# Kernel tuning notes

Hardware: AMD Instinct MI355X
Metric: run time of the kernel (lower is better)

The kernel has to match this reference:

```python
import jax, jax.numpy as jnp
import numpy as np

NUM_CODES = 1024
EMBED_DIM = 256
COMMITMENT_COST = 0.25


def setup_inputs() -> dict:
    key = jax.random.key(0)
    kz, kc = jax.random.split(key)
    z = jax.random.normal(kz, (131072, EMBED_DIM), dtype=jnp.float32)
    # codebook init matches nn.Embedding weight uniform_(-1/num_codes, 1/num_codes)
    codebook = jax.random.uniform(kc, (NUM_CODES, EMBED_DIM), dtype=jnp.float32,
                                  minval=-1.0 / NUM_CODES, maxval=1.0 / NUM_CODES)
    return {"z": z, "codebook": codebook}


def reference(z, codebook):
    # Squared-euclidean distances; argmin is identical to cdist (euclidean) argmin.
    z2 = jnp.sum(z * z, axis=-1, keepdims=True)            # [N, 1]
    c2 = jnp.sum(codebook * codebook, axis=-1)             # [K]
    d = z2 - 2.0 * (z @ codebook.T) + c2                   # [N, K]
    indices = jnp.argmin(d, axis=-1)                       # [N]
    zq = codebook[indices]                                 # [N, D] embedding lookup

    commitment_loss = COMMITMENT_COST * jnp.mean(
        (jax.lax.stop_gradient(zq) - z) ** 2)
    zq_st = z + jax.lax.stop_gradient(zq - z)              # straight-through
    residual = z - jax.lax.stop_gradient(zq)               # z - z_q.detach()

    counts = jnp.bincount(indices, length=NUM_CODES).astype(jnp.float32)
    avg_probs = counts / jnp.sum(counts)
    perplexity = jnp.exp(-jnp.sum(avg_probs * jnp.log(avg_probs + 1e-10)))

    return zq_st, residual, indices, commitment_loss, perplexity
```

## Files before the change

kernel.cpp:

```cpp
#include <hip/hip_runtime.h>
#include <math.h>

#define NR 131072
#define KC 1024
#define DD 256

#define ZQ_OFF  0
#define RES_OFF 33554432
#define IDX_OFF 67108864
#define LOSS_OFF 67239936
#define PERP_OFF 67239937

#define WS_CNT 0
#define WS_C2N 4096
#define WS_BSS 8192
#define WS_CBS 16384

#define MARG 5e-4f
#define CCAP 24

#define FM(x,y) __fmul_rn((x),(y))
#define FA(x,y) __fadd_rn((x),(y))

typedef __attribute__((ext_vector_type(8))) short bf16x8;
typedef __attribute__((ext_vector_type(4))) float f32x4;

static __device__ __forceinline__ unsigned short bf16h(float f) {
  unsigned int u = __float_as_uint(f);
  u += 0x7FFFu + ((u >> 16) & 1u);
  return (unsigned short)(u >> 16);
}

static __device__ __forceinline__ float np_sumsq128(const float* __restrict__ q) {
  float lane[16];
#pragma unroll
  for (int l = 0; l < 16; l++) {
    float s0 = FM(q[l +   0], q[l +   0]);
    float s1 = FM(q[l +  16], q[l +  16]);
    float s2 = FM(q[l +  32], q[l +  32]);
    float s3 = FM(q[l +  48], q[l +  48]);
    float s4 = FM(q[l +  64], q[l +  64]);
    float s5 = FM(q[l +  80], q[l +  80]);
    float s6 = FM(q[l +  96], q[l +  96]);
    float s7 = FM(q[l + 112], q[l + 112]);
    lane[l] = FA(FA(FA(s0, s1), FA(s2, s3)), FA(FA(s4, s5), FA(s6, s7)));
  }
#pragma unroll
  for (int h = 8; h >= 1; h >>= 1)
#pragma unroll
    for (int l = 0; l < 8; l++)
      if (l < h) lane[l] = FA(lane[l], lane[l + h]);
  return lane[0];
}

static __device__ __forceinline__ float np_sumsq256(const float* __restrict__ p) {
  return FA(np_sumsq128(p), np_sumsq128(p + 128));
}

__global__ void vqs_c2(const float* __restrict__ cb, float* __restrict__ c2n) {
  const int code = blockIdx.x * 256 + threadIdx.x;
  if (code < KC) c2n[code] = np_sumsq256(cb + (size_t)code * DD);
}

__global__ void vqs_cbsplit(const float* __restrict__ cb,
                            unsigned short* __restrict__ cbs) {
  const int g  = blockIdx.x * 256 + threadIdx.x;
  const int t  = g >> 9;
  const int gi = g & 511;
  const int kc = gi >> 6, q = (gi >> 4) & 3, c = gi & 15;
  const float* src = cb + (size_t)(t * 16 + c) * DD + kc * 32 + q * 8;
  unsigned int w[4];
#pragma unroll
  for (int p = 0; p < 4; p++)
    w[p] = (unsigned int)bf16h(src[p * 2]) |
           ((unsigned int)bf16h(src[p * 2 + 1]) << 16);
  *(uint4*)(cbs + (size_t)g * 8) = make_uint4(w[0], w[1], w[2], w[3]);
}

__global__ __launch_bounds__(256, 4) void vqs_main(
    const float* __restrict__ z, const float* __restrict__ cb,
    const unsigned short* __restrict__ cbs,
    const float* __restrict__ c2n,
    float* __restrict__ out, int* __restrict__ counts,
    double* __restrict__ bss) {
  __shared__ unsigned short ccode[128][CCAP];
  __shared__ float cd[128][CCAP];
  __shared__ int ccnt[128];
  __shared__ float m1row[128];
  __shared__ float z2s[128];
  __shared__ int rowidx[128];
  __shared__ __align__(16) float c2l[1024];
  __shared__ double wred[4];

  const int tid = threadIdx.x, wg = blockIdx.x;
  const int wv = tid >> 6, ln = tid & 63;
  const int rl = ln & 15;
  const int qk = ln >> 4;
  const int rowg0 = wg * 128 + wv * 32 + rl;

#pragma unroll
  for (int i = 0; i < 4; i++)
    ((float4*)c2l)[i * 64 + ln] = ((const float4*)c2n)[i * 64 + ln];
  if (ln < 32) ccnt[wv * 32 + ln] = 0;

  bf16x8 zH0[8], zH1[8];
#pragma unroll
  for (int kc = 0; kc < 8; kc++) {
    const float4* p0 = (const float4*)(z + (size_t)rowg0 * DD + kc * 32 + qk * 8);
    const float4* p1 = (const float4*)(z + (size_t)(rowg0 + 16) * DD + kc * 32 + qk * 8);
    const float4 a0 = p0[0], b0 = p0[1];
    const float4 a1 = p1[0], b1 = p1[1];
    zH0[kc][0] = (short)bf16h(a0.x); zH0[kc][1] = (short)bf16h(a0.y);
    zH0[kc][2] = (short)bf16h(a0.z); zH0[kc][3] = (short)bf16h(a0.w);
    zH0[kc][4] = (short)bf16h(b0.x); zH0[kc][5] = (short)bf16h(b0.y);
    zH0[kc][6] = (short)bf16h(b0.z); zH0[kc][7] = (short)bf16h(b0.w);
    zH1[kc][0] = (short)bf16h(a1.x); zH1[kc][1] = (short)bf16h(a1.y);
    zH1[kc][2] = (short)bf16h(a1.z); zH1[kc][3] = (short)bf16h(a1.w);
    zH1[kc][4] = (short)bf16h(b1.x); zH1[kc][5] = (short)bf16h(b1.y);
    zH1[kc][6] = (short)bf16h(b1.z); zH1[kc][7] = (short)bf16h(b1.w);
  }

  {
    const int gg = ln >> 4, l = ln & 15;
#pragma unroll 1
    for (int g4 = 0; g4 < 8; g4++) {
      const int rlcl = wv * 32 + g4 * 4 + gg;
      const float* q = z + (size_t)(wg * 128 + rlcl) * DD;
      float blk[2];
#pragma unroll
      for (int b = 0; b < 2; b++) {
        const float* qq = q + b * 128;
        const float s0 = FM(qq[l +   0], qq[l +   0]);
        const float s1 = FM(qq[l +  16], qq[l +  16]);
        const float s2 = FM(qq[l +  32], qq[l +  32]);
        const float s3 = FM(qq[l +  48], qq[l +  48]);
        const float s4 = FM(qq[l +  64], qq[l +  64]);
        const float s5 = FM(qq[l +  80], qq[l +  80]);
        const float s6 = FM(qq[l +  96], qq[l +  96]);
        const float s7 = FM(qq[l + 112], qq[l + 112]);
        float v = FA(FA(FA(s0, s1), FA(s2, s3)), FA(FA(s4, s5), FA(s6, s7)));
#pragma unroll
        for (int h = 8; h >= 1; h >>= 1) v = FA(v, __shfl_down(v, h, 16));
        blk[b] = v;
      }
      if (l == 0) z2s[rlcl] = FA(blk[0], blk[1]);
    }
  }

  const float z2v0 = z2s[wv * 32 + rl];
  const float z2v1 = z2s[wv * 32 + rl + 16];
  const int rw0 = wv * 32 + rl;

  float m10 = INFINITY, m11 = INFINITY;
#pragma unroll 2
  for (int t = 0; t < 64; t++) {
    bf16x8 aH[8];
#pragma unroll
    for (int kc = 0; kc < 8; kc++)
      aH[kc] = *(const bf16x8*)(cbs + (size_t)t * 4096 + kc * 512 + ln * 8);

    f32x4 accA = {0.f, 0.f, 0.f, 0.f}, accB = accA;
#pragma unroll
    for (int kc = 0; kc < 8; kc++) {
      accA = __builtin_amdgcn_mfma_f32_16x16x32_bf16(aH[kc], zH0[kc], accA, 0, 0, 0);
      accB = __builtin_amdgcn_mfma_f32_16x16x32_bf16(aH[kc], zH1[kc], accB, 0, 0, 0);
    }
    const float4 c2v4 = *(const float4*)&c2l[t * 16 + qk * 4];
    float dh0[4], dh1[4];
#pragma unroll
    for (int r = 0; r < 4; r++) {
      const float c2v = r == 0 ? c2v4.x : r == 1 ? c2v4.y : r == 2 ? c2v4.z : c2v4.w;
      dh0[r] = z2v0 - 2.f * accA[r] + c2v;
      dh1[r] = z2v1 - 2.f * accB[r] + c2v;
      m10 = fminf(m10, dh0[r]);
      m11 = fminf(m11, dh1[r]);
    }
    m10 = fminf(m10, __shfl_xor(m10, 16));
    m10 = fminf(m10, __shfl_xor(m10, 32));
    m11 = fminf(m11, __shfl_xor(m11, 16));
    m11 = fminf(m11, __shfl_xor(m11, 32));
#pragma unroll
    for (int r = 0; r < 4; r++) {
      if (dh0[r] <= m10 + MARG) {
        const int s = atomicAdd(&ccnt[rw0], 1);
        if (s < CCAP) {
          ccode[rw0][s] = (unsigned short)(t * 16 + qk * 4 + r);
          cd[rw0][s] = dh0[r];
        }
      }
      if (dh1[r] <= m11 + MARG) {
        const int s = atomicAdd(&ccnt[rw0 + 16], 1);
        if (s < CCAP) {
          ccode[rw0 + 16][s] = (unsigned short)(t * 16 + qk * 4 + r);
          cd[rw0 + 16][s] = dh1[r];
        }
      }
    }
  }

  if (qk == 0) { m1row[rw0] = m10; m1row[rw0 + 16] = m11; }

  if (ln < 32) {
    const int rwl = wv * 32 + ln;
    const int row = wg * 128 + rwl;
    const float mf = m1row[rwl] + MARG;
    const int nc = ccnt[rwl];
    int best;
    if (nc > CCAP) {
      const float* zr = z + (size_t)row * DD;
      const float z2r = z2s[rwl];
      float db = INFINITY; best = 0;
      for (int c = 0; c < KC; c++) {
        const float* cr = cb + (size_t)c * DD;
        float dot = 0.f;
#pragma unroll 8
        for (int k = 0; k < DD; k++) dot = __fmaf_rn(zr[k], cr[k], dot);
        const float t1 = 2.0f * dot;
        const float d = FA(FA(z2r, -t1), c2l[c]);
        if (d < db) { db = d; best = c; }
      }
    } else {
      int kept = 0, kcode = 0;
      for (int s = 0; s < nc; s++)
        if (cd[rwl][s] <= mf) { kept++; kcode = ccode[rwl][s]; }
      if (kept == 1) best = kcode;
      else {
        const float* zr = z + (size_t)row * DD;
        const float z2r = z2s[rwl];
        float db = INFINITY; int bi = 0x7FFFFFFF;
        for (int s = 0; s < nc; s++) {
          if (cd[rwl][s] > mf) continue;
          const int c = ccode[rwl][s];
          const float* cr = cb + (size_t)c * DD;
          float dot = 0.f;
#pragma unroll 8
          for (int k = 0; k < DD; k++) dot = __fmaf_rn(zr[k], cr[k], dot);
          const float t1 = 2.0f * dot;
          const float d = FA(FA(z2r, -t1), c2l[c]);
          if (d < db || (d == db && c < bi)) { db = d; bi = c; }
        }
        best = bi;
      }
    }
    rowidx[rwl] = best;
    atomicAdd(&counts[best], 1);
    out[IDX_OFF + row] = (float)best;
  }

  float ss = 0.f;
#pragma unroll 1
  for (int g = 0; g < 32; g += 8) {
    float4 r4b[8], q4b[8];
#pragma unroll
    for (int u = 0; u < 8; u++) {
      const int rlcl = wv * 32 + g + u;
      const size_t zrow = (size_t)(wg * 128 + rlcl) * DD;
      r4b[u] = ((const float4*)(z + zrow))[ln];
      q4b[u] = ((const float4*)(cb + (size_t)rowidx[rlcl] * DD))[ln];
    }
#pragma unroll
    for (int u = 0; u < 8; u++) {
      const int rlcl = wv * 32 + g + u;
      const size_t zrow = (size_t)(wg * 128 + rlcl) * DD;
      const float4 r4 = r4b[u];
      const float4 q4 = q4b[u];
      float4 stv, rsv; float dq;
      stv.x = r4.x + (q4.x - r4.x); rsv.x = r4.x - q4.x; dq = q4.x - r4.x; ss = fmaf(dq, dq, ss);
      stv.y = r4.y + (q4.y - r4.y); rsv.y = r4.y - q4.y; dq = q4.y - r4.y; ss = fmaf(dq, dq, ss);
      stv.z = r4.z + (q4.z - r4.z); rsv.z = r4.z - q4.z; dq = q4.z - r4.z; ss = fmaf(dq, dq, ss);
      stv.w = r4.w + (q4.w - r4.w); rsv.w = r4.w - q4.w; dq = q4.w - r4.w; ss = fmaf(dq, dq, ss);
      ((float4*)(out + ZQ_OFF  + zrow))[ln] = stv;
      ((float4*)(out + RES_OFF + zrow))[ln] = rsv;
    }
  }
  double dss = (double)ss;
  for (int o = 32; o; o >>= 1) dss += __shfl_down(dss, o, 64);
  if (ln == 0) wred[wv] = dss;
  __syncthreads();
  if (tid == 0) bss[wg] = wred[0] + wred[1] + wred[2] + wred[3];
}

__global__ void vqs_final(const int* __restrict__ counts,
                          const double* __restrict__ bss,
                          float* __restrict__ out) {
  __shared__ double red[256];
  const int t = threadIdx.x;
  double s = 0.0;
  for (int i = t; i < 1024; i += 256) s += bss[i];
  red[t] = s; __syncthreads();
  for (int s2 = 128; s2 > 0; s2 >>= 1) { if (t < s2) red[t] += red[t + s2]; __syncthreads(); }
  const double ssq = red[0];
  __syncthreads();
  double h = 0.0;
  for (int c = t; c < 1024; c += 256) {
    double p = (double)counts[c] / 131072.0;
    h += p * log(p + 1e-10);
  }
  red[t] = h; __syncthreads();
  for (int s2 = 128; s2 > 0; s2 >>= 1) { if (t < s2) red[t] += red[t + s2]; __syncthreads(); }
  if (t == 0) {
    out[LOSS_OFF] = (float)(0.25 * ssq / 33554432.0);
    out[PERP_OFF] = (float)exp(-red[0]);
  }
}

extern "C" void kernel_launch(void* const* d_in, const int* in_sizes, int n_in,
                              void* d_out, int out_size, void* d_ws, size_t ws_size,
                              hipStream_t stream) {
  const float* z;
  const float* cb;
  if (in_sizes[0] == NR * DD) { z = (const float*)d_in[0]; cb = (const float*)d_in[1]; }
  else                        { cb = (const float*)d_in[0]; z = (const float*)d_in[1]; }

  float* out = (float*)d_out;
  char* ws = (char*)d_ws;
  int*            counts = (int*)(ws + WS_CNT);
  float*          c2n    = (float*)(ws + WS_C2N);
  double*         bssp   = (double*)(ws + WS_BSS);
  unsigned short* cbs    = (unsigned short*)(ws + WS_CBS);

  hipMemsetAsync(counts, 0, 4096, stream);
  vqs_c2<<<4, 256, 0, stream>>>(cb, c2n);
  vqs_cbsplit<<<128, 256, 0, stream>>>(cb, cbs);
  vqs_main<<<NR / 128, 256, 0, stream>>>(z, cb, cbs, c2n, out, counts, bssp);
  vqs_final<<<1, 256, 0, stream>>>(counts, bssp, out);
}
```

Measured before the change: 305.5 us.

## Split output writing into a separate kernel after index computation

Moves the straight-through/residual output writes and the squared-error reduction out of the main distance/argmin kernel into a new kernel launched with 2048 blocks, passing indices through a workspace buffer. The aim is to keep the main kernel lean on registers and LDS, and to let the bandwidth-heavy store phase run at higher occupancy on its own. The cost is that z is read a second time from memory, plus an extra launch and an index round-trip.

```diff
diff --git a/kernel.cpp b/kernel.cpp
--- a/kernel.cpp
+++ b/kernel.cpp
@@ -13,8 +13,9 @@
 
 #define WS_CNT 0
 #define WS_C2N 4096
-#define WS_BSS 8192
-#define WS_CBS 16384
+#define WS_IDX 8192
+#define WS_BSS 532480
+#define WS_CBS 548864
 
 #define MARG 5e-4f
 #define CCAP 24
@@ -57,12 +58,12 @@
   return FA(np_sumsq128(p), np_sumsq128(p + 128));
 }
 
-__global__ void vqs_c2(const float* __restrict__ cb, float* __restrict__ c2n) {
+__global__ void vqt_c2(const float* __restrict__ cb, float* __restrict__ c2n) {
   const int code = blockIdx.x * 256 + threadIdx.x;
   if (code < KC) c2n[code] = np_sumsq256(cb + (size_t)code * DD);
 }
 
-__global__ void vqs_cbsplit(const float* __restrict__ cb,
+__global__ void vqt_cbsplit(const float* __restrict__ cb,
                             unsigned short* __restrict__ cbs) {
   const int g  = blockIdx.x * 256 + threadIdx.x;
   const int t  = g >> 9;
@@ -77,20 +78,18 @@
   *(uint4*)(cbs + (size_t)g * 8) = make_uint4(w[0], w[1], w[2], w[3]);
 }
 
-__global__ __launch_bounds__(256, 4) void vqs_main(
+__global__ __launch_bounds__(256, 4) void vqt_main(
     const float* __restrict__ z, const float* __restrict__ cb,
     const unsigned short* __restrict__ cbs,
     const float* __restrict__ c2n,
     float* __restrict__ out, int* __restrict__ counts,
-    double* __restrict__ bss) {
+    int* __restrict__ idxw) {
   __shared__ unsigned short ccode[128][CCAP];
   __shared__ float cd[128][CCAP];
   __shared__ int ccnt[128];
   __shared__ float m1row[128];
   __shared__ float z2s[128];
-  __shared__ int rowidx[128];
   __shared__ __align__(16) float c2l[1024];
-  __shared__ double wred[4];
 
   const int tid = threadIdx.x, wg = blockIdx.x;
   const int wv = tid >> 6, ln = tid & 63;
@@ -242,26 +241,33 @@
         best = bi;
       }
     }
-    rowidx[rwl] = best;
     atomicAdd(&counts[best], 1);
+    idxw[row] = best;
     out[IDX_OFF + row] = (float)best;
   }
+}
+
+__global__ __launch_bounds__(256) void vqt_out(
+    const float* __restrict__ z, const float* __restrict__ cb,
+    const int* __restrict__ idxw, float* __restrict__ out,
+    double* __restrict__ bss) {
+  __shared__ double wred[4];
+  const int wv = threadIdx.x >> 6, ln = threadIdx.x & 63;
+  const int rowbase = (blockIdx.x * 4 + wv) * 16;
 
   float ss = 0.f;
 #pragma unroll 1
-  for (int g = 0; g < 32; g += 8) {
+  for (int g = 0; g < 16; g += 8) {
     float4 r4b[8], q4b[8];
 #pragma unroll
     for (int u = 0; u < 8; u++) {
-      const int rlcl = wv * 32 + g + u;
-      const size_t zrow = (size_t)(wg * 128 + rlcl) * DD;
+      const size_t zrow = (size_t)(rowbase + g + u) * DD;
       r4b[u] = ((const float4*)(z + zrow))[ln];
-      q4b[u] = ((const float4*)(cb + (size_t)rowidx[rlcl] * DD))[ln];
+      q4b[u] = ((const float4*)(cb + (size_t)idxw[rowbase + g + u] * DD))[ln];
     }
 #pragma unroll
     for (int u = 0; u < 8; u++) {
-      const int rlcl = wv * 32 + g + u;
-      const size_t zrow = (size_t)(wg * 128 + rlcl) * DD;
+      const size_t zrow = (size_t)(rowbase + g + u) * DD;
       const float4 r4 = r4b[u];
       const float4 q4 = q4b[u];
       float4 stv, rsv; float dq;
@@ -277,16 +283,16 @@
   for (int o = 32; o; o >>= 1) dss += __shfl_down(dss, o, 64);
   if (ln == 0) wred[wv] = dss;
   __syncthreads();
-  if (tid == 0) bss[wg] = wred[0] + wred[1] + wred[2] + wred[3];
-}
-
-__global__ void vqs_final(const int* __restrict__ counts,
+  if (threadIdx.x == 0) bss[blockIdx.x] = wred[0] + wred[1] + wred[2] + wred[3];
+}
+
+__global__ void vqt_final(const int* __restrict__ counts,
                           const double* __restrict__ bss,
                           float* __restrict__ out) {
   __shared__ double red[256];
   const int t = threadIdx.x;
   double s = 0.0;
-  for (int i = t; i < 1024; i += 256) s += bss[i];
+  for (int i = t; i < 2048; i += 256) s += bss[i];
   red[t] = s; __syncthreads();
   for (int s2 = 128; s2 > 0; s2 >>= 1) { if (t < s2) red[t] += red[t + s2]; __syncthreads(); }
   const double ssq = red[0];
@@ -316,12 +322,14 @@
   char* ws = (char*)d_ws;
   int*            counts = (int*)(ws + WS_CNT);
   float*          c2n    = (float*)(ws + WS_C2N);
+  int*            idxw   = (int*)(ws + WS_IDX);
   double*         bssp   = (double*)(ws + WS_BSS);
   unsigned short* cbs    = (unsigned short*)(ws + WS_CBS);
 
   hipMemsetAsync(counts, 0, 4096, stream);
-  vqs_c2<<<4, 256, 0, stream>>>(cb, c2n);
-  vqs_cbsplit<<<128, 256, 0, stream>>>(cb, cbs);
-  vqs_main<<<NR / 128, 256, 0, stream>>>(z, cb, cbs, c2n, out, counts, bssp);
-  vqs_final<<<1, 256, 0, stream>>>(counts, bssp, out);
-}
+  vqt_c2<<<4, 256, 0, stream>>>(cb, c2n);
+  vqt_cbsplit<<<128, 256, 0, stream>>>(cb, cbs);
+  vqt_main<<<NR / 128, 256, 0, stream>>>(z, cb, cbs, c2n, out, counts, idxw);
+  vqt_out<<<2048, 256, 0, stream>>>(z, cb, idxw, out, bssp);
+  vqt_final<<<1, 256, 0, stream>>>(counts, bssp, out);
+}
```

Result: slower. 333.2 us (+9.0%).

## Double-buffer codebook tiles in LDS via async global_load_lds

Applied to the files above, without the earlier changes.

Codebook bf16 tiles are prefetched one iteration ahead into per-wave double-buffered LDS using global_load_lds, with explicit vmcnt waits, instead of loading directly into registers each iteration. Launch bounds drop to one block per SIMD-group target and the loop is no longer unrolled. The intent is to hide L2 latency of codebook fetches behind MFMA work. It costs 64 KB of extra LDS per block, which sharply lowers occupancy.

```diff
diff --git a/kernel.cpp b/kernel.cpp
--- a/kernel.cpp
+++ b/kernel.cpp
@@ -29,6 +29,12 @@
   unsigned int u = __float_as_uint(f);
   u += 0x7FFFu + ((u >> 16) & 1u);
   return (unsigned short)(u >> 16);
+}
+
+static __device__ __forceinline__ void glds16(const void* g, void* l) {
+  __builtin_amdgcn_global_load_lds(
+      (const __attribute__((address_space(1))) void*)g,
+      (__attribute__((address_space(3))) void*)l, 16, 0, 0);
 }
 
 static __device__ __forceinline__ float np_sumsq128(const float* __restrict__ q) {
@@ -57,12 +63,12 @@
   return FA(np_sumsq128(p), np_sumsq128(p + 128));
 }
 
-__global__ void vqs_c2(const float* __restrict__ cb, float* __restrict__ c2n) {
+__global__ void vqA_c2(const float* __restrict__ cb, float* __restrict__ c2n) {
   const int code = blockIdx.x * 256 + threadIdx.x;
   if (code < KC) c2n[code] = np_sumsq256(cb + (size_t)code * DD);
 }
 
-__global__ void vqs_cbsplit(const float* __restrict__ cb,
+__global__ void vqA_cbsplit(const float* __restrict__ cb,
                             unsigned short* __restrict__ cbs) {
   const int g  = blockIdx.x * 256 + threadIdx.x;
   const int t  = g >> 9;
@@ -77,12 +83,13 @@
   *(uint4*)(cbs + (size_t)g * 8) = make_uint4(w[0], w[1], w[2], w[3]);
 }
 
-__global__ __launch_bounds__(256, 4) void vqs_main(
+__global__ __launch_bounds__(256, 1) void vqA_main(
     const float* __restrict__ z, const float* __restrict__ cb,
     const unsigned short* __restrict__ cbs,
     const float* __restrict__ c2n,
     float* __restrict__ out, int* __restrict__ counts,
     double* __restrict__ bss) {
+  __shared__ __align__(16) unsigned short ct[4][2][4096];
   __shared__ unsigned short ccode[128][CCAP];
   __shared__ float cd[128][CCAP];
   __shared__ int ccnt[128];
@@ -97,6 +104,16 @@
   const int rl = ln & 15;
   const int qk = ln >> 4;
   const int rowg0 = wg * 128 + wv * 32 + rl;
+
+#define STG(T, B) do {                                                        \
+    _Pragma("unroll")                                                         \
+    for (int kc_ = 0; kc_ < 8; kc_++) {                                       \
+      glds16(cbs + (size_t)(T) * 4096 + kc_ * 512 + ln * 8,                   \
+             &ct[wv][B][kc_ * 512]);                                          \
+    }                                                                         \
+  } while (0)
+
+  STG(0, 0);
 
 #pragma unroll
   for (int i = 0; i < 4; i++)
@@ -152,18 +169,23 @@
   const int rw0 = wv * 32 + rl;
 
   float m10 = INFINITY, m11 = INFINITY;
-#pragma unroll 2
+#pragma unroll 1
   for (int t = 0; t < 64; t++) {
-    bf16x8 aH[8];
-#pragma unroll
-    for (int kc = 0; kc < 8; kc++)
-      aH[kc] = *(const bf16x8*)(cbs + (size_t)t * 4096 + kc * 512 + ln * 8);
-
+    if (t < 63) {
+      STG(t + 1, (t + 1) & 1);
+      asm volatile("s_waitcnt vmcnt(8)" ::: "memory");
+    } else {
+      asm volatile("s_waitcnt vmcnt(0)" ::: "memory");
+    }
+    __builtin_amdgcn_sched_barrier(0);
+
+    const unsigned short* cbuf = &ct[wv][t & 1][0];
     f32x4 accA = {0.f, 0.f, 0.f, 0.f}, accB = accA;
 #pragma unroll
     for (int kc = 0; kc < 8; kc++) {
-      accA = __builtin_amdgcn_mfma_f32_16x16x32_bf16(aH[kc], zH0[kc], accA, 0, 0, 0);
-      accB = __builtin_amdgcn_mfma_f32_16x16x32_bf16(aH[kc], zH1[kc], accB, 0, 0, 0);
+      const bf16x8 aH = *(const bf16x8*)&cbuf[kc * 512 + ln * 8];
+      accA = __builtin_amdgcn_mfma_f32_16x16x32_bf16(aH, zH0[kc], accA, 0, 0, 0);
+      accB = __builtin_amdgcn_mfma_f32_16x16x32_bf16(aH, zH1[kc], accB, 0, 0, 0);
     }
     const float4 c2v4 = *(const float4*)&c2l[t * 16 + qk * 4];
     float dh0[4], dh1[4];
@@ -197,6 +219,7 @@
       }
     }
   }
+#undef STG
 
   if (qk == 0) { m1row[rw0] = m10; m1row[rw0 + 16] = m11; }
 
@@ -280,7 +303,7 @@
   if (tid == 0) bss[wg] = wred[0] + wred[1] + wred[2] + wred[3];
 }
 
-__global__ void vqs_final(const int* __restrict__ counts,
+__global__ void vqA_final(const int* __restrict__ counts,
                           const double* __restrict__ bss,
                           float* __restrict__ out) {
   __shared__ double red[256];
@@ -320,8 +343,8 @@
   unsigned short* cbs    = (unsigned short*)(ws + WS_CBS);
 
   hipMemsetAsync(counts, 0, 4096, stream);
-  vqs_c2<<<4, 256, 0, stream>>>(cb, c2n);
-  vqs_cbsplit<<<128, 256, 0, stream>>>(cb, cbs);
-  vqs_main<<<NR / 128, 256, 0, stream>>>(z, cb, cbs, c2n, out, counts, bssp);
-  vqs_final<<<1, 256, 0, stream>>>(counts, bssp, out);
-}
+  vqA_c2<<<4, 256, 0, stream>>>(cb, c2n);
+  vqA_cbsplit<<<128, 256, 0, stream>>>(cb, cbs);
+  vqA_main<<<NR / 128, 256, 0, stream>>>(z, cb, cbs, c2n, out, counts, bssp);
+  vqA_final<<<1, 256, 0, stream>>>(counts, bssp, out);
+}
```

After: 481.0 us. 57.4% more time.
